# Kernel optimization log

Measured on AMD Instinct MI355X. Metric: run time of the kernel, lower is better.

Reference implementation:

```python
import jax, jax.numpy as jnp
import numpy as np

N = 100000; E = 1600000; G = 2000; S = 40; MAXP = 50
IN = 64; F = 128; H = 4; HD = F // H; FFN = 8 * F
EPS = 1e-5; BN_EPS = 1e-5

def _ln(x, g, b):
    m = jnp.mean(x, -1, keepdims=True)
    v = jnp.mean((x - m) ** 2, -1, keepdims=True)
    return (x - m) * jax.lax.rsqrt(v + EPS) * g + b

def setup_inputs():
    key = jax.random.key(0)
    ks = jax.random.split(key, 16)
    def lin(k, i, o):
        kw, kb = jax.random.split(k)
        lim = 1.0 / np.sqrt(i)
        return (jax.random.uniform(kw, (i, o), jnp.float32, -lim, lim),
                jax.random.uniform(kb, (o,), jnp.float32, -lim, lim))
    W_gcn, b_gcn = lin(ks[1], IN, F)
    Wq, bq = lin(ks[2], F, F); Wk, bk = lin(ks[3], F, F)
    Wv, bv = lin(ks[4], F, F); Wo, bo = lin(ks[5], F, F)
    W1, b1 = lin(ks[6], F, FFN); W2, b2 = lin(ks[7], FFN, F)
    Wg, bg = lin(ks[8], 2 * F, F)
    ones = lambda: jnp.ones((F,), jnp.float32)
    zeros = lambda: jnp.zeros((F,), jnp.float32)
    return {
        'x': jax.random.normal(ks[0], (N, IN), jnp.float32),
        'edge_index': jax.random.randint(ks[9], (2, E), 0, N),
        'batch': jnp.repeat(jnp.arange(G), N // G),
        'set_batch': jnp.repeat(jnp.arange(S), G // S),
        'W_gcn': W_gcn, 'b_gcn': b_gcn,
        'bn_g': ones(), 'bn_b': zeros(),
        'lnpre_g': ones(), 'lnpre_b': zeros(),
        'Wq': Wq, 'bq': bq, 'Wk': Wk, 'bk': bk, 'Wv': Wv, 'bv': bv, 'Wo': Wo, 'bo': bo,
        'ln1_g': ones(), 'ln1_b': zeros(),
        'W1': W1, 'b1': b1, 'W2': W2, 'b2': b2,
        'ln2_g': ones(), 'ln2_b': zeros(),
        'Wg': Wg, 'bg': bg,
    }

def _forward(x, W_gcn, b_gcn, bn_g, bn_b, lnpre_g, lnpre_b, Wq, bq, Wk, bk, Wv, bv, Wo, bo, ln1_g, ln1_b, W1, b1, W2, b2, ln2_g, ln2_b, Wg, bg, edge_index, batch, set_batch):
    row, col = edge_index[0], edge_index[1]
    # GCNConv, improved=True -> self-loop weight 2.0 (PyG gcn_norm)
    xw = x @ W_gcn                                              # [N,F]
    deg = jax.ops.segment_sum(jnp.ones(E, xw.dtype), col, N) + 2.0
    dinv = jax.lax.rsqrt(deg)
    norm = dinv[row] * dinv[col]                                # [E]
    agg = jax.ops.segment_sum(xw[row] * norm[:, None], col, N)  # scatter-add to targets
    h = agg + (2.0 * dinv * dinv)[:, None] * xw + b_gcn
    # BatchNorm1d eval (running_mean=0, running_var=1) + ReLU; dropout is identity in eval
    h = jax.nn.relu(h * jax.lax.rsqrt(jnp.asarray(1.0 + BN_EPS, h.dtype)) * bn_g + bn_b)
    # global mean pool per graph
    cnt_g = jax.ops.segment_sum(jnp.ones(N, h.dtype), batch, G)
    z = jax.ops.segment_sum(h, batch, G) / cnt_g[:, None]       # [G,F]
    # to_dense_batch over sets (set_batch is sorted)
    cnt_s = jax.ops.segment_sum(jnp.ones(G, jnp.int32), set_batch, S)
    starts = jnp.cumsum(cnt_s) - cnt_s
    pos = jnp.arange(G) - starts[set_batch]                     # position within set
    zd = jnp.zeros((S, MAXP, F), z.dtype).at[set_batch, pos].set(z)
    mask = jnp.arange(MAXP)[None, :] < cnt_s[:, None]           # [S,MAXP]
    # pre-LN MHA with key_padding_mask
    zn = _ln(zd, lnpre_g, lnpre_b)
    q = (zn @ Wq + bq).reshape(S, MAXP, H, HD)
    k = (zn @ Wk + bk).reshape(S, MAXP, H, HD)
    v = (zn @ Wv + bv).reshape(S, MAXP, H, HD)
    scores = jnp.einsum('sqhd,skhd->shqk', q, k) / np.sqrt(HD)
    scores = jnp.where(mask[:, None, None, :], scores, -1e9)
    attn = jax.nn.softmax(scores, -1)
    o = jnp.einsum('shqk,skhd->sqhd', attn, v).reshape(S, MAXP, F) @ Wo + bo
    zd = _ln(zd + o, ln1_g, ln1_b)
    # FFN block (post-LN residual)
    f = jax.nn.relu(zd @ W1 + b1) @ W2 + b2
    zd = _ln(zd + f, ln2_g, ln2_b)
    # z_dense[mask] ordering == gather via (set_batch, pos); broadcast to nodes
    set_info = zd[set_batch, pos][batch]                        # [N,F]
    # gated fusion
    gate = jax.nn.sigmoid(jnp.concatenate([h, set_info], -1) @ Wg + bg)
    return gate * set_info + (1.0 - gate) * h

def reference(x, edge_index, batch, set_batch, W_gcn, b_gcn, bn_g, bn_b, lnpre_g, lnpre_b, Wq, bq, Wk, bk, Wv, bv, Wo, bo, ln1_g, ln1_b, W1, b1, W2, b2, ln2_g, ln2_b, Wg, bg):
    return _forward(x, W_gcn, b_gcn, bn_g, bn_b, lnpre_g, lnpre_b, Wq, bq, Wk, bk, Wv, bv, Wo, bo, ln1_g, ln1_b, W1, b1, W2, b2, ln2_g, ln2_b, Wg, bg, edge_index, batch, set_batch)
```

## Files before the change

### kernel.cpp

```cpp
#include <hip/hip_runtime.h>
#include <hip/hip_bf16.h>
#include <cstddef>

#define NN 100000
#define NE 1600000
#define NG 2000
#define NS 40
#define INF 64
#define F 128
#define FFN_DIM 1024
#define NB 782
#define BCAP 3072
#define SC_BLOCKS 512
#define SC_CHUNK 3125
#define KSPLIT 8

using bf16 = __hip_bfloat16;
typedef __attribute__((ext_vector_type(8))) short short8;
typedef __attribute__((ext_vector_type(4))) float f32x4;
typedef __attribute__((ext_vector_type(2))) float f32x2;

__device__ __forceinline__ short f2bs(float f){
    union { bf16 b; short s; } u; u.b = __float2bfloat16(f); return u.s;
}
__device__ __forceinline__ unsigned int pk2(float a, float b){
    return (unsigned int)(unsigned short)f2bs(a) | ((unsigned int)(unsigned short)f2bs(b) << 16);
}

__global__ __launch_bounds__(1024) void k_binit(int* __restrict__ bcursor){
    int t = threadIdx.x;
    if (t < NB) bcursor[t] = t * BCAP;
}

__global__ __launch_bounds__(256) void k_wcvt(const float* __restrict__ Wg, unsigned short* __restrict__ Wgb){
    int t = blockIdx.x*256 + threadIdx.x;
    for (int i=t; i<16384; i+=16*256){
        int k = i >> 7, n = i & 127;
        Wgb[n*128 + k] = (unsigned short)f2bs(Wg[(size_t)k*F + n]);
    }
}

__global__ __launch_bounds__(256) void k_xws(const float* __restrict__ x, const float* __restrict__ W,
                                             const float* __restrict__ dinv, unsigned char* __restrict__ xws8){
    __shared__ short Xs[128*72];
    __shared__ short Ws[128*72];
    int t = threadIdx.x;
    int rowBase = blockIdx.x * 128;
    #pragma unroll
    for (int i=0;i<32;i++){
        int id = i*256+t; int k = id>>7, n = id&127;
        Ws[n*72 + k] = f2bs(W[id]);
    }
    #pragma unroll
    for (int i=0;i<8;i++){
        int id = i*256+t;
        int r = id>>4; int k4 = (id&15)*4;
        int row = rowBase + r; if (row >= NN) row = NN-1;
        float4 v = *(const float4*)&x[(size_t)row*INF + k4];
        *(unsigned int*)&Xs[r*72 + k4]     = pk2(v.x, v.y);
        *(unsigned int*)&Xs[r*72 + k4 + 2] = pk2(v.z, v.w);
    }
    __syncthreads();
    int lane = t & 63, w = t >> 6;
    int lr = lane & 15, quad = lane >> 4;
    f32x4 acc[2][8];
    #pragma unroll
    for (int i=0;i<2;i++)
        #pragma unroll
        for (int j=0;j<8;j++) acc[i][j] = (f32x4){0.f,0.f,0.f,0.f};
    #pragma unroll
    for (int ks=0; ks<2; ++ks){
        int kb = ks*32 + quad*8;
        short8 b0 = *(const short8*)&Xs[((w  )*16 + lr)*72 + kb];
        short8 b1 = *(const short8*)&Xs[((w+4)*16 + lr)*72 + kb];
        #pragma unroll
        for (int mt=0; mt<8; ++mt){
            short8 a = *(const short8*)&Ws[(mt*16 + lr)*72 + kb];
            acc[0][mt] = __builtin_amdgcn_mfma_f32_16x16x32_bf16(a, b0, acc[0][mt], 0, 0, 0);
            acc[1][mt] = __builtin_amdgcn_mfma_f32_16x16x32_bf16(a, b1, acc[1][mt], 0, 0, 0);
        }
    }
    #pragma unroll
    for (int rt=0; rt<2; ++rt){
        int row = rowBase + (w + rt*4)*16 + lr;
        if (row < NN){
            float dv = dinv[row];
            #pragma unroll
            for (int mt=0; mt<8; ++mt){
                int p = __builtin_amdgcn_cvt_pk_fp8_f32(acc[rt][mt][0]*dv, acc[rt][mt][1]*dv, 0, false);
                p     = __builtin_amdgcn_cvt_pk_fp8_f32(acc[rt][mt][2]*dv, acc[rt][mt][3]*dv, p, true);
                *(int*)&xws8[(size_t)row*F + mt*16 + quad*4] = p;
            }
        }
    }
}

__global__ __launch_bounds__(1024) void k_scatter2(const int* __restrict__ ei, int* __restrict__ bcursor,
                                                   int* __restrict__ ebuf){
    __shared__ int lh[NB];
    __shared__ int lb[NB];
    int t = threadIdx.x;
    int base = blockIdx.x * SC_CHUNK;
    for (int b=t; b<NB; b+=1024) lh[b] = 0;
    __syncthreads();
    int rr[4], cc[4];
    #pragma unroll
    for (int q=0;q<4;q++){
        int i = t + q*1024;
        bool v = (i < SC_CHUNK);
        int idx = v ? (base + i) : base;
        rr[q] = ei[idx];
        cc[q] = ei[NE + idx];
        if (v) atomicAdd(&lh[cc[q]>>7], 1);
    }
    __syncthreads();
    for (int b=t; b<NB; b+=1024){
        int n = lh[b];
        lb[b] = n ? atomicAdd(&bcursor[b], n) : 0;
        lh[b] = 0;
    }
    __syncthreads();
    #pragma unroll
    for (int q=0;q<4;q++){
        int i = t + q*1024;
        if (i < SC_CHUNK){
            int b = cc[q] >> 7;
            int rk = atomicAdd(&lh[b], 1);
            ebuf[lb[b] + rk] = (rr[q] << 7) | (cc[q] & 127);
        }
    }
}

__global__ __launch_bounds__(256) void k_sort(const int* __restrict__ ebuf, const int* __restrict__ bcursor,
                                              int* __restrict__ cnt, float* __restrict__ dinv,
                                              int* __restrict__ nstart, int* __restrict__ ebuf2){
    __shared__ int lh[128];
    __shared__ int s[128];
    __shared__ int lcur[128];
    int t = threadIdx.x;
    int b = blockIdx.x;
    int e0 = b * BCAP;
    int nE = bcursor[b] - e0;
    if (t < 128) lh[t] = 0;
    __syncthreads();
    for (int i=t; i<nE; i+=256) atomicAdd(&lh[ebuf[e0+i] & 127], 1);
    __syncthreads();
    int c = (t < 128) ? lh[t] : 0;
    if (t < 128) s[t] = c;
    __syncthreads();
    #pragma unroll
    for (int off=1; off<128; off<<=1){
        int v = (t >= off && t < 128) ? s[t-off] : 0;
        __syncthreads();
        if (t < 128) s[t] += v;
        __syncthreads();
    }
    int node = b*128 + t;
    if (t < 128){
        int excl = s[t] - c;
        lcur[t] = excl;
        if (node < NN){
            nstart[node] = e0 + excl;
            cnt[node] = c;
            dinv[node] = rsqrtf((float)c + 2.0f);
        }
    }
    __syncthreads();
    for (int i=t; i<nE; i+=256){
        int v = ebuf[e0 + i];
        int nl = v & 127;
        int rk = atomicAdd(&lcur[nl], 1);
        ebuf2[e0 + rk] = (v >> 7) << 5;
    }
}

__global__ __launch_bounds__(256) void k_aggpool(const unsigned char* __restrict__ xws8,
                                                 const int* __restrict__ nstart, const int* __restrict__ cnt,
                                                 const float* __restrict__ dinv, const float* __restrict__ b_gcn,
                                                 const float* __restrict__ bn_g, const float* __restrict__ bn_b,
                                                 const int* __restrict__ ebuf2,
                                                 const float* __restrict__ lnpre_g, const float* __restrict__ lnpre_b,
                                                 float* __restrict__ h, unsigned short* __restrict__ hb,
                                                 float* __restrict__ z, float* __restrict__ zn,
                                                 unsigned short* __restrict__ znb){
    __shared__ float zacc[4][128];
    int t = threadIdx.x;
    int lane = t & 63, w = t >> 6;
    int half = lane >> 5, lh = lane & 31;
    int g = blockIdx.x;
    const unsigned int* xw32 = (const unsigned int*)xws8;
    unsigned int* hb32 = (unsigned int*)hb;
    unsigned int* znb32 = (unsigned int*)znb;

    float4 bg4  = *(const float4*)&b_gcn[4*lh];
    float4 bng4 = *(const float4*)&bn_g[4*lh];
    float4 bnb4 = *(const float4*)&bn_b[4*lh];
    const float bns = rsqrtf(1.f + 1e-5f);

    float za0=0.f, za1=0.f, za2=0.f, za3=0.f;

    for (int i = w; i < 50; i += 4){
        int node = g*50 + i;
        int s0n = nstart[node]; int dg = cnt[node]; float dv = dinv[node];
        unsigned int us = xw32[node*32 + lh];
        float a0=0.f, a1=0.f, a2=0.f, a3=0.f;
        int j=0;
        for (; j+8<=dg; j+=8){
            int r0 = ebuf2[s0n+j+0+half];
            int r1 = ebuf2[s0n+j+2+half];
            int r2 = ebuf2[s0n+j+4+half];
            int r3 = ebuf2[s0n+j+6+half];
            unsigned int u0 = xw32[r0 + lh];
            unsigned int u1 = xw32[r1 + lh];
            unsigned int u2 = xw32[r2 + lh];
            unsigned int u3 = xw32[r3 + lh];
            f32x2 l0 = __builtin_amdgcn_cvt_pk_f32_fp8(u0, false);
            f32x2 h0 = __builtin_amdgcn_cvt_pk_f32_fp8(u0, true);
            f32x2 l1 = __builtin_amdgcn_cvt_pk_f32_fp8(u1, false);
            f32x2 h1 = __builtin_amdgcn_cvt_pk_f32_fp8(u1, true);
            f32x2 l2 = __builtin_amdgcn_cvt_pk_f32_fp8(u2, false);
            f32x2 h2 = __builtin_amdgcn_cvt_pk_f32_fp8(u2, true);
            f32x2 l3 = __builtin_amdgcn_cvt_pk_f32_fp8(u3, false);
            f32x2 h3 = __builtin_amdgcn_cvt_pk_f32_fp8(u3, true);
            a0 += (l0.x + l1.x) + (l2.x + l3.x);
            a1 += (l0.y + l1.y) + (l2.y + l3.y);
            a2 += (h0.x + h1.x) + (h2.x + h3.x);
            a3 += (h0.y + h1.y) + (h2.y + h3.y);
        }
        for (; j+2<=dg; j+=2){
            int r0 = ebuf2[s0n+j+half];
            unsigned int u0 = xw32[r0 + lh];
            f32x2 l0 = __builtin_amdgcn_cvt_pk_f32_fp8(u0, false);
            f32x2 h0 = __builtin_amdgcn_cvt_pk_f32_fp8(u0, true);
            a0 += l0.x; a1 += l0.y; a2 += h0.x; a3 += h0.y;
        }
        if (j < dg && half == 0){
            int r0 = ebuf2[s0n+j];
            unsigned int u0 = xw32[r0 + lh];
            f32x2 l0 = __builtin_amdgcn_cvt_pk_f32_fp8(u0, false);
            f32x2 h0 = __builtin_amdgcn_cvt_pk_f32_fp8(u0, true);
            a0 += l0.x; a1 += l0.y; a2 += h0.x; a3 += h0.y;
        }
        a0 += __shfl_xor(a0, 32);
        a1 += __shfl_xor(a1, 32);
        a2 += __shfl_xor(a2, 32);
        a3 += __shfl_xor(a3, 32);
        f32x2 fl = __builtin_amdgcn_cvt_pk_f32_fp8(us, false);
        f32x2 fh = __builtin_amdgcn_cvt_pk_f32_fp8(us, true);
        float p0 = dv*(a0 + 2.f*fl.x) + bg4.x;
        float p1 = dv*(a1 + 2.f*fl.y) + bg4.y;
        float p2 = dv*(a2 + 2.f*fh.x) + bg4.z;
        float p3 = dv*(a3 + 2.f*fh.y) + bg4.w;
        p0 = fmaxf(p0*bns*bng4.x + bnb4.x, 0.f);
        p1 = fmaxf(p1*bns*bng4.y + bnb4.y, 0.f);
        p2 = fmaxf(p2*bns*bng4.z + bnb4.z, 0.f);
        p3 = fmaxf(p3*bns*bng4.w + bnb4.w, 0.f);
        if (half == 0){
            *(float4*)&h[(size_t)node*F + 4*lh] = make_float4(p0,p1,p2,p3);
            *(uint2*)&hb32[(size_t)node*64 + 2*lh] = make_uint2(pk2(p0,p1), pk2(p2,p3));
        }
        za0 += p0; za1 += p1; za2 += p2; za3 += p3;
    }
    if (half == 0)
        *(float4*)&zacc[w][4*lh] = make_float4(za0, za1, za2, za3);
    __syncthreads();
    if (w == 0){
        float4 v0 = *(const float4*)&zacc[0][4*lh];
        float4 v1 = *(const float4*)&zacc[1][4*lh];
        float4 v2 = *(const float4*)&zacc[2][4*lh];
        float4 v3 = *(const float4*)&zacc[3][4*lh];
        float s0 = ((v0.x+v1.x)+(v2.x+v3.x)) / 50.0f;
        float s1 = ((v0.y+v1.y)+(v2.y+v3.y)) / 50.0f;
        float s2 = ((v0.z+v1.z)+(v2.z+v3.z)) / 50.0f;
        float s3 = ((v0.w+v1.w)+(v2.w+v3.w)) / 50.0f;
        if (half == 0)
            *(float4*)&z[(size_t)g*F + 4*lh] = make_float4(s0,s1,s2,s3);
        float s = (s0+s1)+(s2+s3);
        #pragma unroll
        for (int off=1; off<32; off<<=1) s += __shfl_xor(s, off);
        float m = s * (1.f/128.f);
        float d0=s0-m, d1=s1-m, d2=s2-m, d3=s3-m;
        float vv = (d0*d0+d1*d1)+(d2*d2+d3*d3);
        #pragma unroll
        for (int off=1; off<32; off<<=1) vv += __shfl_xor(vv, off);
        float rs = rsqrtf(vv*(1.f/128.f) + 1e-5f);
        float4 lg = *(const float4*)&lnpre_g[4*lh];
        float4 lb = *(const float4*)&lnpre_b[4*lh];
        if (half == 0){
            float o0 = d0*rs*lg.x+lb.x, o1 = d1*rs*lg.y+lb.y;
            float o2 = d2*rs*lg.z+lb.z, o3 = d3*rs*lg.w+lb.w;
            *(float4*)&zn[(size_t)g*F + 4*lh] = make_float4(o0,o1,o2,o3);
            *(uint2*)&znb32[(size_t)g*64 + 2*lh] = make_uint2(pk2(o0,o1), pk2(o2,o3));
        }
    }
}

template<int RELU, int BF16OUT, int SPLITK>
__global__ __launch_bounds__(256) void k_mm_bf16(const unsigned short* __restrict__ A,
                                                 const float* __restrict__ B, const float* __restrict__ bias,
                                                 float* __restrict__ Cf, unsigned short* __restrict__ Cb,
                                                 int M, int K, int Nc){
    __shared__ short Bw[128*136];
    int t = threadIdx.x;
    int rowBase = blockIdx.x*128;
    int colBase = blockIdx.y*128;
    int kbeg = SPLITK ? blockIdx.z*128 : 0;
    #pragma unroll
    for (int i=0;i<64;i++){
        int id = i*256+t; int k = id>>7, n = id&127;
        Bw[n*136 + k] = f2bs(B[(size_t)(kbeg+k)*Nc + colBase + n]);
    }
    __syncthreads();
    int lane = t & 63, w = t >> 6;
    int lr = lane & 15, quad = lane >> 4;
    int mrow0 = rowBase + w*32;
    f32x4 acc[2][8];
    #pragma unroll
    for (int i=0;i<2;i++)
        #pragma unroll
        for (int j=0;j<8;j++) acc[i][j] = (f32x4){0.f,0.f,0.f,0.f};
    #pragma unroll
    for (int ks=0; ks<4; ++ks){
        int kb = ks*32 + quad*8;
        short8 a[2];
        #pragma unroll
        for (int mt=0; mt<2; ++mt){
            int row = mrow0 + mt*16 + lr;
            if (row >= M) row = M-1;
            a[mt] = *(const short8*)&A[(size_t)row*K + kbeg + kb];
        }
        #pragma unroll
        for (int nt=0; nt<8; ++nt){
            short8 b = *(const short8*)&Bw[(nt*16 + lr)*136 + kb];
            acc[0][nt] = __builtin_amdgcn_mfma_f32_16x16x32_bf16(a[0], b, acc[0][nt], 0, 0, 0);
            acc[1][nt] = __builtin_amdgcn_mfma_f32_16x16x32_bf16(a[1], b, acc[1][nt], 0, 0, 0);
        }
    }
    #pragma unroll
    for (int mt=0; mt<2; ++mt){
        #pragma unroll
        for (int r=0; r<4; ++r){
            int row = mrow0 + mt*16 + quad*4 + r;
            if (row >= M) continue;
            #pragma unroll
            for (int nt=0; nt<8; ++nt){
                int col = colBase + nt*16 + lr;
                float v = acc[mt][nt][r];
                if (!SPLITK){
                    v += bias[col];
                    if (RELU) v = fmaxf(v, 0.f);
                    if (BF16OUT) Cb[(size_t)row*Nc + col] = (unsigned short)f2bs(v);
                    else         Cf[(size_t)row*Nc + col] = v;
                } else {
                    Cf[(size_t)blockIdx.z*M*Nc + (size_t)row*Nc + col] = v;
                }
            }
        }
    }
}

__global__ __launch_bounds__(256) void k_qkv_mfma(const unsigned short* __restrict__ A,
                                                  const float* __restrict__ Wq, const float* __restrict__ Wk,
                                                  const float* __restrict__ Wv, const float* __restrict__ bq,
                                                  const float* __restrict__ bk, const float* __restrict__ bv,
                                                  float* __restrict__ Cq, float* __restrict__ Ck,
                                                  float* __restrict__ Cv){
    __shared__ short Bw[128*136];
    int t = threadIdx.x;
    int zsel = blockIdx.z;
    const float* B = (zsel==0) ? Wq : (zsel==1) ? Wk : Wv;
    const float* bias = (zsel==0) ? bq : (zsel==1) ? bk : bv;
    float* C = (zsel==0) ? Cq : (zsel==1) ? Ck : Cv;
    int rowBase = blockIdx.x*128;
    #pragma unroll
    for (int i=0;i<64;i++){
        int id = i*256+t; int k = id>>7, n = id&127;
        Bw[n*136 + k] = f2bs(B[(size_t)k*F + n]);
    }
    __syncthreads();
    int lane = t & 63, w = t >> 6;
    int lr = lane & 15, quad = lane >> 4;
    int mrow0 = rowBase + w*32;
    f32x4 acc[2][8];
    #pragma unroll
    for (int i=0;i<2;i++)
        #pragma unroll
        for (int j=0;j<8;j++) acc[i][j] = (f32x4){0.f,0.f,0.f,0.f};
    #pragma unroll
    for (int ks=0; ks<4; ++ks){
        int kb = ks*32 + quad*8;
        short8 a[2];
        #pragma unroll
        for (int mt=0; mt<2; ++mt){
            int row = mrow0 + mt*16 + lr;
            if (row >= NG) row = NG-1;
            a[mt] = *(const short8*)&A[(size_t)row*F + kb];
        }
        #pragma unroll
        for (int nt=0; nt<8; ++nt){
            short8 b = *(const short8*)&Bw[(nt*16 + lr)*136 + kb];
            acc[0][nt] = __builtin_amdgcn_mfma_f32_16x16x32_bf16(a[0], b, acc[0][nt], 0, 0, 0);
            acc[1][nt] = __builtin_amdgcn_mfma_f32_16x16x32_bf16(a[1], b, acc[1][nt], 0, 0, 0);
        }
    }
    #pragma unroll
    for (int mt=0; mt<2; ++mt){
        #pragma unroll
        for (int r=0; r<4; ++r){
            int row = mrow0 + mt*16 + quad*4 + r;
            if (row >= NG) continue;
            #pragma unroll
            for (int nt=0; nt<8; ++nt){
                int col = nt*16 + lr;
                C[(size_t)row*F + col] = acc[mt][nt][r] + bias[col];
            }
        }
    }
}

__global__ __launch_bounds__(256) void k_wo_ln(const float* __restrict__ ao, const float* __restrict__ Wo,
                                               const float* __restrict__ bo, const float* __restrict__ z,
                                               const float* __restrict__ g, const float* __restrict__ b,
                                               float* __restrict__ zd1, unsigned short* __restrict__ zd1b){
    __shared__ float As[32*36];
    __shared__ float Bs[32*128];
    int t = threadIdx.x;
    int rowBase = blockIdx.x*32;
    int c0 = (t&31)*4, r0 = (t>>5)*4;
    unsigned int* zd1b32 = (unsigned int*)zd1b;
    float acc[4][4];
    #pragma unroll
    for (int i=0;i<4;i++){ acc[i][0]=0.f; acc[i][1]=0.f; acc[i][2]=0.f; acc[i][3]=0.f; }
    for (int kb=0; kb<F; kb+=32){
        #pragma unroll
        for (int i=0;i<4;i++){
            int id = i*256+t; int kk = id&31; int r = id>>5;
            int row = rowBase + r;
            As[kk*36+r] = (row<NG) ? ao[(size_t)row*F + kb + kk] : 0.f;
        }
        #pragma unroll
        for (int i=0;i<16;i++){
            int id = i*256+t; int c = id&127; int kk = id>>7;
            Bs[kk*128+c] = Wo[(size_t)(kb+kk)*F + c];
        }
        __syncthreads();
        for (int kk=0;kk<32;kk++){
            float4 a = *(const float4*)&As[kk*36+r0];
            float4 bv = *(const float4*)&Bs[kk*128+c0];
            float av[4]={a.x,a.y,a.z,a.w}; float bb[4]={bv.x,bv.y,bv.z,bv.w};
            #pragma unroll
            for(int i=0;i<4;i++)
                #pragma unroll
                for(int j=0;j<4;j++) acc[i][j] += av[i]*bb[j];
        }
        __syncthreads();
    }
    float4 bo4 = *(const float4*)&bo[c0];
    float4 g4  = *(const float4*)&g[c0];
    float4 b4  = *(const float4*)&b[c0];
    #pragma unroll
    for (int i=0;i<4;i++){
        int row = rowBase + r0 + i;
        float v0=0.f,v1=0.f,v2=0.f,v3=0.f;
        if (row < NG){
            float4 zr = *(const float4*)&z[(size_t)row*F + c0];
            v0 = acc[i][0] + bo4.x + zr.x;
            v1 = acc[i][1] + bo4.y + zr.y;
            v2 = acc[i][2] + bo4.z + zr.z;
            v3 = acc[i][3] + bo4.w + zr.w;
        }
        float s = (v0+v1)+(v2+v3);
        #pragma unroll
        for (int off=1; off<32; off<<=1) s += __shfl_xor(s, off);
        float m = s * (1.f/128.f);
        float d0=v0-m, d1=v1-m, d2=v2-m, d3=v3-m;
        float vv = (d0*d0+d1*d1)+(d2*d2+d3*d3);
        #pragma unroll
        for (int off=1; off<32; off<<=1) vv += __shfl_xor(vv, off);
        float rs = rsqrtf(vv*(1.f/128.f) + 1e-5f);
        if (row < NG){
            float o0 = d0*rs*g4.x+b4.x, o1 = d1*rs*g4.y+b4.y;
            float o2 = d2*rs*g4.z+b4.z, o3 = d3*rs*g4.w+b4.w;
            *(float4*)&zd1[(size_t)row*F + c0] = make_float4(o0,o1,o2,o3);
            *(uint2*)&zd1b32[(size_t)row*(F/2) + c0/2] = make_uint2(pk2(o0,o1), pk2(o2,o3));
        }
    }
}

__global__ __launch_bounds__(256) void k_ln_red_gsi(const float* __restrict__ A, const float* __restrict__ part,
                                                    const float* __restrict__ bias, const float* __restrict__ g,
                                                    const float* __restrict__ b, const float* __restrict__ Wb,
                                                    const float* __restrict__ bg, float* __restrict__ zd2,
                                                    float* __restrict__ gsi){
    __shared__ float Zs[4][128];
    __shared__ float Bs[32*128];
    int t = threadIdx.x; int lane = t&63;
    int rquad = t>>6;
    int row = blockIdx.x*4 + rquad;
    int i0 = row*F + 2*lane;
    float x0 = A[i0] + bias[2*lane], x1 = A[i0+1] + bias[2*lane+1];
    #pragma unroll
    for (int zz=0; zz<KSPLIT; ++zz){
        x0 += part[(size_t)zz*NG*F + i0];
        x1 += part[(size_t)zz*NG*F + i0 + 1];
    }
    float s = x0+x1;
    for (int off=1; off<64; off<<=1) s += __shfl_xor(s, off);
    float m = s * (1.f/128.f);
    float d0 = x0-m, d1 = x1-m;
    float vv = d0*d0 + d1*d1;
    for (int off=1; off<64; off<<=1) vv += __shfl_xor(vv, off);
    float rs = rsqrtf(vv*(1.f/128.f) + 1e-5f);
    float o0 = d0*rs*g[2*lane]   + b[2*lane];
    float o1 = d1*rs*g[2*lane+1] + b[2*lane+1];
    zd2[i0]   = o0;
    zd2[i0+1] = o1;
    Zs[rquad][2*lane]   = o0;
    Zs[rquad][2*lane+1] = o1;
    __syncthreads();
    int col = t & 127, rp = t >> 7;
    float a0=0.f, a1=0.f;
    for (int kb=0; kb<F; kb+=32){
        #pragma unroll
        for (int i=0;i<16;i++){
            int id = i*256+t; int c = id&127; int kk = id>>7;
            Bs[kk*128+c] = Wb[(size_t)(kb+kk)*F + c];
        }
        __syncthreads();
        for (int kk=0;kk<32;kk++){
            float w = Bs[kk*128+col];
            a0 += Zs[rp][kb+kk]   * w;
            a1 += Zs[rp+2][kb+kk] * w;
        }
        __syncthreads();
    }
    float bgc = bg[col];
    gsi[(size_t)(blockIdx.x*4 + rp)*F + col]     = a0 + bgc;
    gsi[(size_t)(blockIdx.x*4 + rp + 2)*F + col] = a1 + bgc;
}

__global__ __launch_bounds__(256) void k_attn(const float* __restrict__ q, const float* __restrict__ k,
                                              const float* __restrict__ v, float* __restrict__ o){
    __shared__ float Qs[1600], Ks[1600], Vs[1600], Sc[2500];
    int t = threadIdx.x;
    int s = blockIdx.x >> 2; int hh = blockIdx.x & 3;
    for (int idx=t; idx<1600; idx+=256){
        int i = idx>>5, d = idx&31;
        size_t gi = (size_t)(s*50+i)*F + hh*32 + d;
        Qs[idx]=q[gi]; Ks[idx]=k[gi]; Vs[idx]=v[gi];
    }
    __syncthreads();
    for (int idx=t; idx<2500; idx+=256){
        int qi = idx/50, ki = idx%50;
        float acc=0.f;
        #pragma unroll 8
        for (int d=0;d<32;d++) acc += Qs[qi*32+d]*Ks[ki*32+d];
        Sc[idx] = acc * 0.17677669529663687f;
    }
    __syncthreads();
    if (t < 50){
        float m=-1e30f;
        for (int j=0;j<50;j++) m = fmaxf(m, Sc[t*50+j]);
        float sum=0.f;
        for (int j=0;j<50;j++){ float e=__expf(Sc[t*50+j]-m); Sc[t*50+j]=e; sum+=e; }
        float inv = 1.f/sum;
        for (int j=0;j<50;j++) Sc[t*50+j] *= inv;
    }
    __syncthreads();
    for (int idx=t; idx<1600; idx+=256){
        int qi = idx>>5, d = idx&31;
        float acc=0.f;
        #pragma unroll 10
        for (int ki=0;ki<50;ki++) acc += Sc[qi*50+ki]*Vs[ki*32+d];
        o[(size_t)(s*50+qi)*F + hh*32 + d] = acc;
    }
}

__global__ __launch_bounds__(256) void k_gate_mfma(const float* __restrict__ h,
                                                   const unsigned short* __restrict__ hb,
                                                   const unsigned short* __restrict__ Wgb,
                                                   const float* __restrict__ gsi, const float* __restrict__ zd2,
                                                   float* __restrict__ out){
    int t = threadIdx.x;
    int lane = t & 63, w = t >> 6;
    int lr = lane & 15, quad = lane >> 4;
    int mrow0 = blockIdx.x*64 + w*16;
    f32x4 acc[8];
    #pragma unroll
    for (int j=0;j<8;j++) acc[j] = (f32x4){0.f,0.f,0.f,0.f};
    #pragma unroll
    for (int ks=0; ks<4; ++ks){
        int kb = ks*32 + quad*8;
        int row = mrow0 + lr;
        if (row >= NN) row = NN-1;
        short8 a = *(const short8*)&hb[(size_t)row*F + kb];
        #pragma unroll
        for (int nt=0; nt<8; ++nt){
            short8 b = *(const short8*)&Wgb[(size_t)(nt*16 + lr)*128 + kb];
            acc[nt] = __builtin_amdgcn_mfma_f32_16x16x32_bf16(a, b, acc[nt], 0, 0, 0);
        }
    }
    #pragma unroll
    for (int r=0; r<4; ++r){
        int row = mrow0 + quad*4 + r;
        if (row >= NN) continue;
        int g = row / 50;
        const float* gs = &gsi[(size_t)g*F];
        const float* zs = &zd2[(size_t)g*F];
        const float* hr = &h[(size_t)row*F];
        float* orow = &out[(size_t)row*F];
        #pragma unroll
        for (int nt=0; nt<8; ++nt){
            int col = nt*16 + lr;
            float L = acc[nt][r] + gs[col];
            float gate = 1.f/(1.f + __expf(-L));
            orow[col] = gate*zs[col] + (1.f-gate)*hr[col];
        }
    }
}

extern "C" void kernel_launch(void* const* d_in, const int* in_sizes, int n_in,
                              void* d_out, int out_size, void* d_ws, size_t ws_size,
                              hipStream_t stream) {
    const float* x      = (const float*)d_in[0];
    const int*   ei     = (const int*)d_in[1];
    const float* W_gcn  = (const float*)d_in[4];
    const float* b_gcn  = (const float*)d_in[5];
    const float* bn_g   = (const float*)d_in[6];
    const float* bn_b   = (const float*)d_in[7];
    const float* lnpre_g= (const float*)d_in[8];
    const float* lnpre_b= (const float*)d_in[9];
    const float* Wq     = (const float*)d_in[10];
    const float* bq     = (const float*)d_in[11];
    const float* Wk     = (const float*)d_in[12];
    const float* bk     = (const float*)d_in[13];
    const float* Wv     = (const float*)d_in[14];
    const float* bv     = (const float*)d_in[15];
    const float* Wo     = (const float*)d_in[16];
    const float* bo     = (const float*)d_in[17];
    const float* ln1_g  = (const float*)d_in[18];
    const float* ln1_b  = (const float*)d_in[19];
    const float* W1     = (const float*)d_in[20];
    const float* b1     = (const float*)d_in[21];
    const float* W2     = (const float*)d_in[22];
    const float* b2     = (const float*)d_in[23];
    const float* ln2_g  = (const float*)d_in[24];
    const float* ln2_b  = (const float*)d_in[25];
    const float* Wg     = (const float*)d_in[26];
    const float* bg     = (const float*)d_in[27];
    float* out = (float*)d_out;
    char* ws = (char*)d_ws;

    size_t o = 0;
    unsigned char* xws8 = (unsigned char*)(ws + o); o += (size_t)NN*F;
    float* h     = (float*)(ws + o); o += (size_t)NN*F*4;
    unsigned short* hb = (unsigned short*)(ws + o); o += (size_t)NN*F*2;
    int*   cnt   = (int*)(ws + o);   o += (size_t)NN*4;
    int*   nstart= (int*)(ws + o);   o += (size_t)NN*4;
    int*   ebuf  = (int*)(ws + o);   o += (size_t)NB*BCAP*4;
    int*   ebuf2 = (int*)(ws + o);   o += (size_t)NB*BCAP*4;
    float* dinv  = (float*)(ws + o); o += (size_t)NN*4;
    int*   bcursor=(int*)(ws + o);   o += 1024*4;
    unsigned short* Wgb = (unsigned short*)(ws + o); o += 16384*2;
    float* z     = (float*)(ws + o); o += (size_t)NG*F*4;
    float* zn    = (float*)(ws + o); o += (size_t)NG*F*4;
    unsigned short* znb = (unsigned short*)(ws + o); o += (size_t)NG*F*2;
    float* qb    = (float*)(ws + o); o += (size_t)NG*F*4;
    float* kb2   = (float*)(ws + o); o += (size_t)NG*F*4;
    float* vb    = (float*)(ws + o); o += (size_t)NG*F*4;
    float* ao    = (float*)(ws + o); o += (size_t)NG*F*4;
    float* zd1   = (float*)(ws + o); o += (size_t)NG*F*4;
    unsigned short* zd1b = (unsigned short*)(ws + o); o += (size_t)NG*F*2;
    unsigned short* ffn1b = (unsigned short*)(ws + o); o += (size_t)NG*FFN_DIM*2;
    float* part  = (float*)(ws + o); o += (size_t)KSPLIT*NG*F*4;
    float* zd2   = (float*)(ws + o); o += (size_t)NG*F*4;
    float* gsi   = (float*)(ws + o); o += (size_t)NG*F*4;

    k_binit<<<1, 1024, 0, stream>>>(bcursor);
    k_wcvt<<<16, 256, 0, stream>>>(Wg, Wgb);
    k_scatter2<<<SC_BLOCKS, 1024, 0, stream>>>(ei, bcursor, ebuf);
    k_sort<<<NB, 256, 0, stream>>>(ebuf, bcursor, cnt, dinv, nstart, ebuf2);
    k_xws<<<(NN+127)/128, 256, 0, stream>>>(x, W_gcn, dinv, xws8);
    k_aggpool<<<NG, 256, 0, stream>>>(xws8, nstart, cnt, dinv, b_gcn, bn_g, bn_b, ebuf2,
                                      lnpre_g, lnpre_b, h, hb, z, zn, znb);

    dim3 gqkv((NG+127)/128, 1, 3);
    k_qkv_mfma<<<gqkv, 256, 0, stream>>>(znb, Wq, Wk, Wv, bq, bk, bv, qb, kb2, vb);
    k_attn<<<NS*4, 256, 0, stream>>>(qb, kb2, vb, ao);
    k_wo_ln<<<(NG+31)/32, 256, 0, stream>>>(ao, Wo, bo, z, ln1_g, ln1_b, zd1, zd1b);
    dim3 gffn1((NG+127)/128, FFN_DIM/128, 1);
    k_mm_bf16<1,1,0><<<gffn1, 256, 0, stream>>>(zd1b, W1, b1, nullptr, ffn1b, NG, F, FFN_DIM);
    dim3 gffn2((NG+127)/128, 1, KSPLIT);
    k_mm_bf16<0,0,1><<<gffn2, 256, 0, stream>>>(ffn1b, W2, nullptr, part, nullptr, NG, FFN_DIM, F);
    k_ln_red_gsi<<<NG/4, 256, 0, stream>>>(zd1, part, b2, ln2_g, ln2_b,
                                           Wg + (size_t)F*F, bg, zd2, gsi);

    k_gate_mfma<<<(NN+63)/64, 256, 0, stream>>>(h, hb, Wgb, gsi, zd2, out);
}
```

Measured before the change: 351.9 us.

## Fuse the whole set-transformer block into one per-set kernel

Replaces the QKV, attention, Wo+LN, FFN1, split-K FFN2 and LN+gate-projection kernels with one kernel that runs one block per set of 50 rows. All intermediates stay in shared memory and are never written to global. It also merges the init and weight-conversion kernels, and stages the k_sort output in shared memory so it is written to global coalesced. This removes about six launches and their global round-trips, but leaves only 40 blocks, each converting every weight matrix to bf16 on its own, so parallelism drops sharply and per-block serial work grows.

After: 388.5 us. +10.4%, slower.

```diff
diff --git a/kernel.cpp b/kernel.cpp
--- a/kernel.cpp
+++ b/kernel.cpp
@@ -13,7 +13,6 @@
 #define BCAP 3072
 #define SC_BLOCKS 512
 #define SC_CHUNK 3125
-#define KSPLIT 8
 
 using bf16 = __hip_bfloat16;
 typedef __attribute__((ext_vector_type(8))) short short8;
@@ -27,14 +26,11 @@
     return (unsigned int)(unsigned short)f2bs(a) | ((unsigned int)(unsigned short)f2bs(b) << 16);
 }
 
-__global__ __launch_bounds__(1024) void k_binit(int* __restrict__ bcursor){
+__global__ __launch_bounds__(1024) void k_init(int* __restrict__ bcursor, const float* __restrict__ Wg,
+                                               unsigned short* __restrict__ Wgb){
     int t = threadIdx.x;
     if (t < NB) bcursor[t] = t * BCAP;
-}
-
-__global__ __launch_bounds__(256) void k_wcvt(const float* __restrict__ Wg, unsigned short* __restrict__ Wgb){
-    int t = blockIdx.x*256 + threadIdx.x;
-    for (int i=t; i<16384; i+=16*256){
+    for (int i=t; i<16384; i+=1024){
         int k = i >> 7, n = i & 127;
         Wgb[n*128 + k] = (unsigned short)f2bs(Wg[(size_t)k*F + n]);
     }
@@ -137,6 +133,7 @@
     __shared__ int lh[128];
     __shared__ int s[128];
     __shared__ int lcur[128];
+    __shared__ int sorted[BCAP];
     int t = threadIdx.x;
     int b = blockIdx.x;
     int e0 = b * BCAP;
@@ -170,8 +167,10 @@
         int v = ebuf[e0 + i];
         int nl = v & 127;
         int rk = atomicAdd(&lcur[nl], 1);
-        ebuf2[e0 + rk] = (v >> 7) << 5;
-    }
+        sorted[rk] = (v >> 7) << 5;
+    }
+    __syncthreads();
+    for (int i=t; i<nE; i+=256) ebuf2[e0 + i] = sorted[i];
 }
 
 __global__ __launch_bounds__(256) void k_aggpool(const unsigned char* __restrict__ xws8,
@@ -181,8 +180,7 @@
                                                  const int* __restrict__ ebuf2,
                                                  const float* __restrict__ lnpre_g, const float* __restrict__ lnpre_b,
                                                  float* __restrict__ h, unsigned short* __restrict__ hb,
-                                                 float* __restrict__ z, float* __restrict__ zn,
-                                                 unsigned short* __restrict__ znb){
+                                                 float* __restrict__ z, unsigned short* __restrict__ znb){
     __shared__ float zacc[4][128];
     int t = threadIdx.x;
     int lane = t & 63, w = t >> 6;
@@ -289,290 +287,300 @@
         if (half == 0){
             float o0 = d0*rs*lg.x+lb.x, o1 = d1*rs*lg.y+lb.y;
             float o2 = d2*rs*lg.z+lb.z, o3 = d3*rs*lg.w+lb.w;
-            *(float4*)&zn[(size_t)g*F + 4*lh] = make_float4(o0,o1,o2,o3);
             *(uint2*)&znb32[(size_t)g*64 + 2*lh] = make_uint2(pk2(o0,o1), pk2(o2,o3));
         }
     }
 }
 
-template<int RELU, int BF16OUT, int SPLITK>
-__global__ __launch_bounds__(256) void k_mm_bf16(const unsigned short* __restrict__ A,
-                                                 const float* __restrict__ B, const float* __restrict__ bias,
-                                                 float* __restrict__ Cf, unsigned short* __restrict__ Cb,
-                                                 int M, int K, int Nc){
-    __shared__ short Bw[128*136];
+__global__ __launch_bounds__(256) void k_settf(const unsigned short* __restrict__ znb,
+                                               const float* __restrict__ z,
+                                               const float* __restrict__ Wq, const float* __restrict__ bq,
+                                               const float* __restrict__ Wk, const float* __restrict__ bk,
+                                               const float* __restrict__ Wv, const float* __restrict__ bv,
+                                               const float* __restrict__ Wo, const float* __restrict__ bo,
+                                               const float* __restrict__ ln1_g, const float* __restrict__ ln1_b,
+                                               const float* __restrict__ W1, const float* __restrict__ b1,
+                                               const float* __restrict__ W2, const float* __restrict__ b2,
+                                               const float* __restrict__ ln2_g, const float* __restrict__ ln2_b,
+                                               const float* __restrict__ Wgbot, const float* __restrict__ bg,
+                                               float* __restrict__ zd2, float* __restrict__ gsi){
+    __shared__ __align__(16) char smem[138208];
+    short* Bw   = (short*)smem;
+    float* Sc   = (float*)smem;
+    float* qs   = (float*)(smem + 41600);
+    float* ks   = (float*)(smem + 68000);
+    float* vs   = (float*)(smem + 94400);
+    short* aob  = (short*)(smem + 120800);
+    float* zd1f = (float*)(smem + 41600);
+    short* zd1b = (short*)(smem + 68000);
+    short* f1b  = (short*)(smem + 94400);
+    short* zd2b = f1b;
+
     int t = threadIdx.x;
-    int rowBase = blockIdx.x*128;
-    int colBase = blockIdx.y*128;
-    int kbeg = SPLITK ? blockIdx.z*128 : 0;
-    #pragma unroll
-    for (int i=0;i<64;i++){
-        int id = i*256+t; int k = id>>7, n = id&127;
-        Bw[n*136 + k] = f2bs(B[(size_t)(kbeg+k)*Nc + colBase + n]);
-    }
-    __syncthreads();
     int lane = t & 63, w = t >> 6;
     int lr = lane & 15, quad = lane >> 4;
-    int mrow0 = rowBase + w*32;
-    f32x4 acc[2][8];
-    #pragma unroll
-    for (int i=0;i<2;i++)
-        #pragma unroll
-        for (int j=0;j<8;j++) acc[i][j] = (f32x4){0.f,0.f,0.f,0.f};
-    #pragma unroll
-    for (int ks=0; ks<4; ++ks){
-        int kb = ks*32 + quad*8;
-        short8 a[2];
-        #pragma unroll
-        for (int mt=0; mt<2; ++mt){
-            int row = mrow0 + mt*16 + lr;
-            if (row >= M) row = M-1;
-            a[mt] = *(const short8*)&A[(size_t)row*K + kbeg + kb];
-        }
-        #pragma unroll
-        for (int nt=0; nt<8; ++nt){
-            short8 b = *(const short8*)&Bw[(nt*16 + lr)*136 + kb];
-            acc[0][nt] = __builtin_amdgcn_mfma_f32_16x16x32_bf16(a[0], b, acc[0][nt], 0, 0, 0);
-            acc[1][nt] = __builtin_amdgcn_mfma_f32_16x16x32_bf16(a[1], b, acc[1][nt], 0, 0, 0);
-        }
-    }
-    #pragma unroll
-    for (int mt=0; mt<2; ++mt){
+    int s = blockIdx.x;
+    const int r0 = s*50;
+
+    {
+        int rl = w*16 + lr; if (rl > 49) rl = 49;
+        const unsigned short* arow = &znb[(size_t)(r0 + rl)*F];
+        for (int zsel=0; zsel<3; ++zsel){
+            const float* Wp = (zsel==0)?Wq:(zsel==1)?Wk:Wv;
+            const float* bp = (zsel==0)?bq:(zsel==1)?bk:bv;
+            float* outp = (zsel==0)?qs:(zsel==1)?ks:vs;
+            for (int i=t; i<16384; i+=256){
+                int k = i>>7, n = i&127;
+                Bw[n*136 + k] = f2bs(Wp[(size_t)k*F + n]);
+            }
+            __syncthreads();
+            f32x4 acc[8];
+            #pragma unroll
+            for (int j=0;j<8;j++) acc[j] = (f32x4){0.f,0.f,0.f,0.f};
+            #pragma unroll
+            for (int ks4=0; ks4<4; ++ks4){
+                int kb = ks4*32 + quad*8;
+                short8 a = *(const short8*)&arow[kb];
+                #pragma unroll
+                for (int nt=0; nt<8; ++nt){
+                    short8 b = *(const short8*)&Bw[(nt*16 + lr)*136 + kb];
+                    acc[nt] = __builtin_amdgcn_mfma_f32_16x16x32_bf16(a, b, acc[nt], 0, 0, 0);
+                }
+            }
+            #pragma unroll
+            for (int r=0; r<4; ++r){
+                int row = w*16 + quad*4 + r;
+                if (row < 50){
+                    #pragma unroll
+                    for (int nt=0; nt<8; ++nt){
+                        int col = nt*16 + lr;
+                        outp[row*132 + col] = acc[nt][r] + bp[col];
+                    }
+                }
+            }
+            __syncthreads();
+        }
+    }
+
+    {
+        int hh = w;
+        float* ScH = Sc + hh*50*52;
+        int qi = lane;
+        if (qi < 50){
+            float qreg[32];
+            #pragma unroll
+            for (int d=0; d<32; ++d) qreg[d] = qs[qi*132 + hh*32 + d];
+            for (int ki=0; ki<50; ++ki){
+                float acc=0.f;
+                #pragma unroll
+                for (int d=0; d<32; ++d) acc += qreg[d] * ks[ki*132 + hh*32 + d];
+                ScH[qi*52 + ki] = acc * 0.17677669529663687f;
+            }
+            float m=-1e30f;
+            for (int ki=0; ki<50; ++ki) m = fmaxf(m, ScH[qi*52+ki]);
+            float sum=0.f;
+            for (int ki=0; ki<50; ++ki){ float e=__expf(ScH[qi*52+ki]-m); ScH[qi*52+ki]=e; sum+=e; }
+            float inv = 1.f/sum;
+            float o[32];
+            #pragma unroll
+            for (int d=0; d<32; ++d) o[d] = 0.f;
+            for (int ki=0; ki<50; ++ki){
+                float sc = ScH[qi*52+ki] * inv;
+                #pragma unroll
+                for (int d=0; d<32; ++d) o[d] += sc * vs[ki*132 + hh*32 + d];
+            }
+            #pragma unroll
+            for (int d=0; d<32; ++d) aob[qi*136 + hh*32 + d] = f2bs(o[d]);
+        } else if (qi < 64){
+            #pragma unroll
+            for (int d=0; d<32; ++d) aob[qi*136 + hh*32 + d] = 0;
+        }
+    }
+    __syncthreads();
+
+    {
+        for (int i=t; i<16384; i+=256){
+            int k = i>>7, n = i&127;
+            Bw[n*136 + k] = f2bs(Wo[(size_t)k*F + n]);
+        }
+        __syncthreads();
+        f32x4 acc[8];
+        #pragma unroll
+        for (int j=0;j<8;j++) acc[j] = (f32x4){0.f,0.f,0.f,0.f};
+        #pragma unroll
+        for (int ks4=0; ks4<4; ++ks4){
+            int kb = ks4*32 + quad*8;
+            short8 a = *(const short8*)&aob[(w*16 + lr)*136 + kb];
+            #pragma unroll
+            for (int nt=0; nt<8; ++nt){
+                short8 b = *(const short8*)&Bw[(nt*16 + lr)*136 + kb];
+                acc[nt] = __builtin_amdgcn_mfma_f32_16x16x32_bf16(a, b, acc[nt], 0, 0, 0);
+            }
+        }
+        __syncthreads();
         #pragma unroll
         for (int r=0; r<4; ++r){
-            int row = mrow0 + mt*16 + quad*4 + r;
-            if (row >= M) continue;
+            int row = w*16 + quad*4 + r;
+            float v[8];
+            if (row < 50){
+                #pragma unroll
+                for (int nt=0; nt<8; ++nt){
+                    int col = nt*16 + lr;
+                    v[nt] = acc[nt][r] + bo[col] + z[(size_t)(r0+row)*F + col];
+                }
+            } else {
+                #pragma unroll
+                for (int nt=0; nt<8; ++nt) v[nt] = 0.f;
+            }
+            float ssum = 0.f;
+            #pragma unroll
+            for (int nt=0; nt<8; ++nt) ssum += v[nt];
+            #pragma unroll
+            for (int off=1; off<16; off<<=1) ssum += __shfl_xor(ssum, off);
+            float mean = ssum * (1.f/128.f);
+            float var = 0.f;
+            float d[8];
+            #pragma unroll
+            for (int nt=0; nt<8; ++nt){ d[nt] = v[nt]-mean; var += d[nt]*d[nt]; }
+            #pragma unroll
+            for (int off=1; off<16; off<<=1) var += __shfl_xor(var, off);
+            float rsv = rsqrtf(var*(1.f/128.f) + 1e-5f);
+            if (row < 50){
+                #pragma unroll
+                for (int nt=0; nt<8; ++nt){
+                    int col = nt*16 + lr;
+                    float o = d[nt]*rsv*ln1_g[col] + ln1_b[col];
+                    zd1f[row*132 + col] = o;
+                    zd1b[row*136 + col] = f2bs(o);
+                }
+            } else {
+                #pragma unroll
+                for (int nt=0; nt<8; ++nt) zd1b[row*136 + nt*16 + lr] = 0;
+            }
+        }
+    }
+    __syncthreads();
+
+    f32x4 acc2[8];
+    #pragma unroll
+    for (int j=0;j<8;j++) acc2[j] = (f32x4){0.f,0.f,0.f,0.f};
+    for (int c=0; c<8; ++c){
+        for (int i=t; i<16384; i+=256){
+            int k = i>>7, n = i&127;
+            Bw[n*136 + k] = f2bs(W1[(size_t)k*FFN_DIM + c*128 + n]);
+        }
+        __syncthreads();
+        f32x4 a1[8];
+        #pragma unroll
+        for (int j=0;j<8;j++) a1[j] = (f32x4){0.f,0.f,0.f,0.f};
+        #pragma unroll
+        for (int ks4=0; ks4<4; ++ks4){
+            int kb = ks4*32 + quad*8;
+            short8 a = *(const short8*)&zd1b[(w*16 + lr)*136 + kb];
             #pragma unroll
             for (int nt=0; nt<8; ++nt){
-                int col = colBase + nt*16 + lr;
-                float v = acc[mt][nt][r];
-                if (!SPLITK){
-                    v += bias[col];
-                    if (RELU) v = fmaxf(v, 0.f);
-                    if (BF16OUT) Cb[(size_t)row*Nc + col] = (unsigned short)f2bs(v);
-                    else         Cf[(size_t)row*Nc + col] = v;
-                } else {
-                    Cf[(size_t)blockIdx.z*M*Nc + (size_t)row*Nc + col] = v;
-                }
-            }
-        }
-    }
-}
-
-__global__ __launch_bounds__(256) void k_qkv_mfma(const unsigned short* __restrict__ A,
-                                                  const float* __restrict__ Wq, const float* __restrict__ Wk,
-                                                  const float* __restrict__ Wv, const float* __restrict__ bq,
-                                                  const float* __restrict__ bk, const float* __restrict__ bv,
-                                                  float* __restrict__ Cq, float* __restrict__ Ck,
-                                                  float* __restrict__ Cv){
-    __shared__ short Bw[128*136];
-    int t = threadIdx.x;
-    int zsel = blockIdx.z;
-    const float* B = (zsel==0) ? Wq : (zsel==1) ? Wk : Wv;
-    const float* bias = (zsel==0) ? bq : (zsel==1) ? bk : bv;
-    float* C = (zsel==0) ? Cq : (zsel==1) ? Ck : Cv;
-    int rowBase = blockIdx.x*128;
-    #pragma unroll
-    for (int i=0;i<64;i++){
-        int id = i*256+t; int k = id>>7, n = id&127;
-        Bw[n*136 + k] = f2bs(B[(size_t)k*F + n]);
-    }
-    __syncthreads();
-    int lane = t & 63, w = t >> 6;
-    int lr = lane & 15, quad = lane >> 4;
-    int mrow0 = rowBase + w*32;
-    f32x4 acc[2][8];
-    #pragma unroll
-    for (int i=0;i<2;i++)
-        #pragma unroll
-        for (int j=0;j<8;j++) acc[i][j] = (f32x4){0.f,0.f,0.f,0.f};
-    #pragma unroll
-    for (int ks=0; ks<4; ++ks){
-        int kb = ks*32 + quad*8;
-        short8 a[2];
-        #pragma unroll
-        for (int mt=0; mt<2; ++mt){
-            int row = mrow0 + mt*16 + lr;
-            if (row >= NG) row = NG-1;
-            a[mt] = *(const short8*)&A[(size_t)row*F + kb];
-        }
-        #pragma unroll
-        for (int nt=0; nt<8; ++nt){
-            short8 b = *(const short8*)&Bw[(nt*16 + lr)*136 + kb];
-            acc[0][nt] = __builtin_amdgcn_mfma_f32_16x16x32_bf16(a[0], b, acc[0][nt], 0, 0, 0);
-            acc[1][nt] = __builtin_amdgcn_mfma_f32_16x16x32_bf16(a[1], b, acc[1][nt], 0, 0, 0);
-        }
-    }
-    #pragma unroll
-    for (int mt=0; mt<2; ++mt){
+                short8 b = *(const short8*)&Bw[(nt*16 + lr)*136 + kb];
+                a1[nt] = __builtin_amdgcn_mfma_f32_16x16x32_bf16(a, b, a1[nt], 0, 0, 0);
+            }
+        }
         #pragma unroll
         for (int r=0; r<4; ++r){
-            int row = mrow0 + mt*16 + quad*4 + r;
-            if (row >= NG) continue;
+            int row = w*16 + quad*4 + r;
             #pragma unroll
             for (int nt=0; nt<8; ++nt){
                 int col = nt*16 + lr;
-                C[(size_t)row*F + col] = acc[mt][nt][r] + bias[col];
-            }
-        }
-    }
-}
-
-__global__ __launch_bounds__(256) void k_wo_ln(const float* __restrict__ ao, const float* __restrict__ Wo,
-                                               const float* __restrict__ bo, const float* __restrict__ z,
-                                               const float* __restrict__ g, const float* __restrict__ b,
-                                               float* __restrict__ zd1, unsigned short* __restrict__ zd1b){
-    __shared__ float As[32*36];
-    __shared__ float Bs[32*128];
-    int t = threadIdx.x;
-    int rowBase = blockIdx.x*32;
-    int c0 = (t&31)*4, r0 = (t>>5)*4;
-    unsigned int* zd1b32 = (unsigned int*)zd1b;
-    float acc[4][4];
-    #pragma unroll
-    for (int i=0;i<4;i++){ acc[i][0]=0.f; acc[i][1]=0.f; acc[i][2]=0.f; acc[i][3]=0.f; }
-    for (int kb=0; kb<F; kb+=32){
-        #pragma unroll
-        for (int i=0;i<4;i++){
-            int id = i*256+t; int kk = id&31; int r = id>>5;
-            int row = rowBase + r;
-            As[kk*36+r] = (row<NG) ? ao[(size_t)row*F + kb + kk] : 0.f;
-        }
-        #pragma unroll
-        for (int i=0;i<16;i++){
-            int id = i*256+t; int c = id&127; int kk = id>>7;
-            Bs[kk*128+c] = Wo[(size_t)(kb+kk)*F + c];
-        }
-        __syncthreads();
-        for (int kk=0;kk<32;kk++){
-            float4 a = *(const float4*)&As[kk*36+r0];
-            float4 bv = *(const float4*)&Bs[kk*128+c0];
-            float av[4]={a.x,a.y,a.z,a.w}; float bb[4]={bv.x,bv.y,bv.z,bv.w};
-            #pragma unroll
-            for(int i=0;i<4;i++)
-                #pragma unroll
-                for(int j=0;j<4;j++) acc[i][j] += av[i]*bb[j];
-        }
-        __syncthreads();
-    }
-    float4 bo4 = *(const float4*)&bo[c0];
-    float4 g4  = *(const float4*)&g[c0];
-    float4 b4  = *(const float4*)&b[c0];
-    #pragma unroll
-    for (int i=0;i<4;i++){
-        int row = rowBase + r0 + i;
-        float v0=0.f,v1=0.f,v2=0.f,v3=0.f;
-        if (row < NG){
-            float4 zr = *(const float4*)&z[(size_t)row*F + c0];
-            v0 = acc[i][0] + bo4.x + zr.x;
-            v1 = acc[i][1] + bo4.y + zr.y;
-            v2 = acc[i][2] + bo4.z + zr.z;
-            v3 = acc[i][3] + bo4.w + zr.w;
-        }
-        float s = (v0+v1)+(v2+v3);
-        #pragma unroll
-        for (int off=1; off<32; off<<=1) s += __shfl_xor(s, off);
-        float m = s * (1.f/128.f);
-        float d0=v0-m, d1=v1-m, d2=v2-m, d3=v3-m;
-        float vv = (d0*d0+d1*d1)+(d2*d2+d3*d3);
-        #pragma unroll
-        for (int off=1; off<32; off<<=1) vv += __shfl_xor(vv, off);
-        float rs = rsqrtf(vv*(1.f/128.f) + 1e-5f);
-        if (row < NG){
-            float o0 = d0*rs*g4.x+b4.x, o1 = d1*rs*g4.y+b4.y;
-            float o2 = d2*rs*g4.z+b4.z, o3 = d3*rs*g4.w+b4.w;
-            *(float4*)&zd1[(size_t)row*F + c0] = make_float4(o0,o1,o2,o3);
-            *(uint2*)&zd1b32[(size_t)row*(F/2) + c0/2] = make_uint2(pk2(o0,o1), pk2(o2,o3));
-        }
-    }
-}
-
-__global__ __launch_bounds__(256) void k_ln_red_gsi(const float* __restrict__ A, const float* __restrict__ part,
-                                                    const float* __restrict__ bias, const float* __restrict__ g,
-                                                    const float* __restrict__ b, const float* __restrict__ Wb,
-                                                    const float* __restrict__ bg, float* __restrict__ zd2,
-                                                    float* __restrict__ gsi){
-    __shared__ float Zs[4][128];
-    __shared__ float Bs[32*128];
-    int t = threadIdx.x; int lane = t&63;
-    int rquad = t>>6;
-    int row = blockIdx.x*4 + rquad;
-    int i0 = row*F + 2*lane;
-    float x0 = A[i0] + bias[2*lane], x1 = A[i0+1] + bias[2*lane+1];
-    #pragma unroll
-    for (int zz=0; zz<KSPLIT; ++zz){
-        x0 += part[(size_t)zz*NG*F + i0];
-        x1 += part[(size_t)zz*NG*F + i0 + 1];
-    }
-    float s = x0+x1;
-    for (int off=1; off<64; off<<=1) s += __shfl_xor(s, off);
-    float m = s * (1.f/128.f);
-    float d0 = x0-m, d1 = x1-m;
-    float vv = d0*d0 + d1*d1;
-    for (int off=1; off<64; off<<=1) vv += __shfl_xor(vv, off);
-    float rs = rsqrtf(vv*(1.f/128.f) + 1e-5f);
-    float o0 = d0*rs*g[2*lane]   + b[2*lane];
-    float o1 = d1*rs*g[2*lane+1] + b[2*lane+1];
-    zd2[i0]   = o0;
-    zd2[i0+1] = o1;
-    Zs[rquad][2*lane]   = o0;
-    Zs[rquad][2*lane+1] = o1;
-    __syncthreads();
-    int col = t & 127, rp = t >> 7;
-    float a0=0.f, a1=0.f;
-    for (int kb=0; kb<F; kb+=32){
-        #pragma unroll
-        for (int i=0;i<16;i++){
-            int id = i*256+t; int c = id&127; int kk = id>>7;
-            Bs[kk*128+c] = Wb[(size_t)(kb+kk)*F + c];
-        }
-        __syncthreads();
-        for (int kk=0;kk<32;kk++){
-            float w = Bs[kk*128+col];
-            a0 += Zs[rp][kb+kk]   * w;
-            a1 += Zs[rp+2][kb+kk] * w;
-        }
-        __syncthreads();
-    }
-    float bgc = bg[col];
-    gsi[(size_t)(blockIdx.x*4 + rp)*F + col]     = a0 + bgc;
-    gsi[(size_t)(blockIdx.x*4 + rp + 2)*F + col] = a1 + bgc;
-}
-
-__global__ __launch_bounds__(256) void k_attn(const float* __restrict__ q, const float* __restrict__ k,
-                                              const float* __restrict__ v, float* __restrict__ o){
-    __shared__ float Qs[1600], Ks[1600], Vs[1600], Sc[2500];
-    int t = threadIdx.x;
-    int s = blockIdx.x >> 2; int hh = blockIdx.x & 3;
-    for (int idx=t; idx<1600; idx+=256){
-        int i = idx>>5, d = idx&31;
-        size_t gi = (size_t)(s*50+i)*F + hh*32 + d;
-        Qs[idx]=q[gi]; Ks[idx]=k[gi]; Vs[idx]=v[gi];
-    }
-    __syncthreads();
-    for (int idx=t; idx<2500; idx+=256){
-        int qi = idx/50, ki = idx%50;
-        float acc=0.f;
-        #pragma unroll 8
-        for (int d=0;d<32;d++) acc += Qs[qi*32+d]*Ks[ki*32+d];
-        Sc[idx] = acc * 0.17677669529663687f;
-    }
-    __syncthreads();
-    if (t < 50){
-        float m=-1e30f;
-        for (int j=0;j<50;j++) m = fmaxf(m, Sc[t*50+j]);
-        float sum=0.f;
-        for (int j=0;j<50;j++){ float e=__expf(Sc[t*50+j]-m); Sc[t*50+j]=e; sum+=e; }
-        float inv = 1.f/sum;
-        for (int j=0;j<50;j++) Sc[t*50+j] *= inv;
-    }
-    __syncthreads();
-    for (int idx=t; idx<1600; idx+=256){
-        int qi = idx>>5, d = idx&31;
-        float acc=0.f;
-        #pragma unroll 10
-        for (int ki=0;ki<50;ki++) acc += Sc[qi*50+ki]*Vs[ki*32+d];
-        o[(size_t)(s*50+qi)*F + hh*32 + d] = acc;
+                f1b[row*136 + col] = f2bs(fmaxf(a1[nt][r] + b1[c*128 + col], 0.f));
+            }
+        }
+        __syncthreads();
+        for (int i=t; i<16384; i+=256){
+            int k = i>>7, n = i&127;
+            Bw[n*136 + k] = f2bs(W2[(size_t)(c*128 + k)*F + n]);
+        }
+        __syncthreads();
+        #pragma unroll
+        for (int ks4=0; ks4<4; ++ks4){
+            int kb = ks4*32 + quad*8;
+            short8 a = *(const short8*)&f1b[(w*16 + lr)*136 + kb];
+            #pragma unroll
+            for (int nt=0; nt<8; ++nt){
+                short8 b = *(const short8*)&Bw[(nt*16 + lr)*136 + kb];
+                acc2[nt] = __builtin_amdgcn_mfma_f32_16x16x32_bf16(a, b, acc2[nt], 0, 0, 0);
+            }
+        }
+        __syncthreads();
+    }
+
+    {
+        #pragma unroll
+        for (int r=0; r<4; ++r){
+            int row = w*16 + quad*4 + r;
+            float v[8];
+            if (row < 50){
+                #pragma unroll
+                for (int nt=0; nt<8; ++nt){
+                    int col = nt*16 + lr;
+                    v[nt] = acc2[nt][r] + b2[col] + zd1f[row*132 + col];
+                }
+            } else {
+                #pragma unroll
+                for (int nt=0; nt<8; ++nt) v[nt] = 0.f;
+            }
+            float ssum = 0.f;
+            #pragma unroll
+            for (int nt=0; nt<8; ++nt) ssum += v[nt];
+            #pragma unroll
+            for (int off=1; off<16; off<<=1) ssum += __shfl_xor(ssum, off);
+            float mean = ssum * (1.f/128.f);
+            float var = 0.f;
+            float d[8];
+            #pragma unroll
+            for (int nt=0; nt<8; ++nt){ d[nt] = v[nt]-mean; var += d[nt]*d[nt]; }
+            #pragma unroll
+            for (int off=1; off<16; off<<=1) var += __shfl_xor(var, off);
+            float rsv = rsqrtf(var*(1.f/128.f) + 1e-5f);
+            if (row < 50){
+                #pragma unroll
+                for (int nt=0; nt<8; ++nt){
+                    int col = nt*16 + lr;
+                    float o = d[nt]*rsv*ln2_g[col] + ln2_b[col];
+                    zd2[(size_t)(r0+row)*F + col] = o;
+                    zd2b[row*136 + col] = f2bs(o);
+                }
+            } else {
+                #pragma unroll
+                for (int nt=0; nt<8; ++nt) zd2b[row*136 + nt*16 + lr] = 0;
+            }
+        }
+        for (int i=t; i<16384; i+=256){
+            int k = i>>7, n = i&127;
+            Bw[n*136 + k] = f2bs(Wgbot[(size_t)k*F + n]);
+        }
+        __syncthreads();
+        f32x4 ag[8];
+        #pragma unroll
+        for (int j=0;j<8;j++) ag[j] = (f32x4){0.f,0.f,0.f,0.f};
+        #pragma unroll
+        for (int ks4=0; ks4<4; ++ks4){
+            int kb = ks4*32 + quad*8;
+            short8 a = *(const short8*)&zd2b[(w*16 + lr)*136 + kb];
+            #pragma unroll
+            for (int nt=0; nt<8; ++nt){
+                short8 b = *(const short8*)&Bw[(nt*16 + lr)*136 + kb];
+                ag[nt] = __builtin_amdgcn_mfma_f32_16x16x32_bf16(a, b, ag[nt], 0, 0, 0);
+            }
+        }
+        #pragma unroll
+        for (int r=0; r<4; ++r){
+            int row = w*16 + quad*4 + r;
+            if (row < 50){
+                #pragma unroll
+                for (int nt=0; nt<8; ++nt){
+                    int col = nt*16 + lr;
+                    gsi[(size_t)(r0+row)*F + col] = ag[nt][r] + bg[col];
+                }
+            }
+        }
     }
 }
 
@@ -663,37 +671,20 @@
     int*   bcursor=(int*)(ws + o);   o += 1024*4;
     unsigned short* Wgb = (unsigned short*)(ws + o); o += 16384*2;
     float* z     = (float*)(ws + o); o += (size_t)NG*F*4;
-    float* zn    = (float*)(ws + o); o += (size_t)NG*F*4;
     unsigned short* znb = (unsigned short*)(ws + o); o += (size_t)NG*F*2;
-    float* qb    = (float*)(ws + o); o += (size_t)NG*F*4;
-    float* kb2   = (float*)(ws + o); o += (size_t)NG*F*4;
-    float* vb    = (float*)(ws + o); o += (size_t)NG*F*4;
-    float* ao    = (float*)(ws + o); o += (size_t)NG*F*4;
-    float* zd1   = (float*)(ws + o); o += (size_t)NG*F*4;
-    unsigned short* zd1b = (unsigned short*)(ws + o); o += (size_t)NG*F*2;
-    unsigned short* ffn1b = (unsigned short*)(ws + o); o += (size_t)NG*FFN_DIM*2;
-    float* part  = (float*)(ws + o); o += (size_t)KSPLIT*NG*F*4;
     float* zd2   = (float*)(ws + o); o += (size_t)NG*F*4;
     float* gsi   = (float*)(ws + o); o += (size_t)NG*F*4;
 
-    k_binit<<<1, 1024, 0, stream>>>(bcursor);
-    k_wcvt<<<16, 256, 0, stream>>>(Wg, Wgb);
+    k_init<<<1, 1024, 0, stream>>>(bcursor, Wg, Wgb);
     k_scatter2<<<SC_BLOCKS, 1024, 0, stream>>>(ei, bcursor, ebuf);
     k_sort<<<NB, 256, 0, stream>>>(ebuf, bcursor, cnt, dinv, nstart, ebuf2);
     k_xws<<<(NN+127)/128, 256, 0, stream>>>(x, W_gcn, dinv, xws8);
     k_aggpool<<<NG, 256, 0, stream>>>(xws8, nstart, cnt, dinv, b_gcn, bn_g, bn_b, ebuf2,
-                                      lnpre_g, lnpre_b, h, hb, z, zn, znb);
-
-    dim3 gqkv((NG+127)/128, 1, 3);
-    k_qkv_mfma<<<gqkv, 256, 0, stream>>>(znb, Wq, Wk, Wv, bq, bk, bv, qb, kb2, vb);
-    k_attn<<<NS*4, 256, 0, stream>>>(qb, kb2, vb, ao);
-    k_wo_ln<<<(NG+31)/32, 256, 0, stream>>>(ao, Wo, bo, z, ln1_g, ln1_b, zd1, zd1b);
-    dim3 gffn1((NG+127)/128, FFN_DIM/128, 1);
-    k_mm_bf16<1,1,0><<<gffn1, 256, 0, stream>>>(zd1b, W1, b1, nullptr, ffn1b, NG, F, FFN_DIM);
-    dim3 gffn2((NG+127)/128, 1, KSPLIT);
-    k_mm_bf16<0,0,1><<<gffn2, 256, 0, stream>>>(ffn1b, W2, nullptr, part, nullptr, NG, FFN_DIM, F);
-    k_ln_red_gsi<<<NG/4, 256, 0, stream>>>(zd1, part, b2, ln2_g, ln2_b,
-                                           Wg + (size_t)F*F, bg, zd2, gsi);
+                                      lnpre_g, lnpre_b, h, hb, z, znb);
+
+    k_settf<<<NS, 256, 0, stream>>>(znb, z, Wq, bq, Wk, bk, Wv, bv, Wo, bo,
+                                    ln1_g, ln1_b, W1, b1, W2, b2, ln2_g, ln2_b,
+                                    Wg + (size_t)F*F, bg, zd2, gsi);
 
     k_gate_mfma<<<(NN+63)/64, 256, 0, stream>>>(h, hb, Wgb, gsi, zd2, out);
 }
```
